# Kernel tuning notes

Hardware: AMD Instinct MI355X
Metric: run time of the kernel (lower is better)

Reference implementation:

```python
import jax, jax.numpy as jnp
import numpy as np

N = 50000
E = 1600000
IN_CH = 128
OUT_CH = 128
NEG_SLOPE = 0.2


def _gat_conv(x, W, att_src, att_dst, bias, src, dst, heads, out_ch, concat):
    # x: [N, F_in], W: [F_in, heads*out_ch], att_*: [heads, out_ch]
    n = x.shape[0]
    h = (x @ W).reshape(n, heads, out_ch)                    # [N, H, C]
    a_src = jnp.einsum('nhc,hc->nh', h, att_src)             # [N, H]
    a_dst = jnp.einsum('nhc,hc->nh', h, att_dst)             # [N, H]
    logits = jax.nn.leaky_relu(a_src[src] + a_dst[dst], NEG_SLOPE)  # [Etot, H]
    m = jax.ops.segment_max(logits, dst, num_segments=n)     # per-dst max (self-loops ensure non-empty)
    e = jnp.exp(logits - m[dst])
    denom = jax.ops.segment_sum(e, dst, num_segments=n)
    alpha = e / denom[dst]                                   # [Etot, H]
    msgs = h[src] * alpha[:, :, None]                        # [Etot, H, C]
    out = jax.ops.segment_sum(msgs, dst, num_segments=n)     # [N, H, C]
    out = out.reshape(n, heads * out_ch) if concat else out.mean(axis=1)
    return out + bias


def setup_inputs() -> dict:
    key = jax.random.key(0)
    ks = jax.random.split(key, 12)
    x = jax.random.normal(ks[0], (N, IN_CH), dtype=jnp.float32)
    edge_index = jax.random.randint(ks[1], (2, E), 0, N, dtype=jnp.int32)
    s = 0.1
    W_map = jax.random.normal(ks[2], (IN_CH, OUT_CH), dtype=jnp.float32) * s
    b_map = jnp.zeros((OUT_CH,), dtype=jnp.float32)
    # conv1: 128 -> 8 per head, 8 heads
    W1 = jax.random.normal(ks[3], (OUT_CH, 64), dtype=jnp.float32) * s
    att_src1 = jax.random.normal(ks[4], (8, 8), dtype=jnp.float32) * s
    att_dst1 = jax.random.normal(ks[5], (8, 8), dtype=jnp.float32) * s
    b1 = jnp.zeros((64,), dtype=jnp.float32)
    # conv2: 64 -> 128, 1 head, concat=False
    W2 = jax.random.normal(ks[6], (64, OUT_CH), dtype=jnp.float32) * s
    att_src2 = jax.random.normal(ks[7], (1, OUT_CH), dtype=jnp.float32) * s
    att_dst2 = jax.random.normal(ks[8], (1, OUT_CH), dtype=jnp.float32) * s
    b2 = jnp.zeros((OUT_CH,), dtype=jnp.float32)
    return {"x": x, "edge_index": edge_index, "W_map": W_map, "b_map": b_map,
            "W1": W1, "att_src1": att_src1, "att_dst1": att_dst1, "b1": b1,
            "W2": W2, "att_src2": att_src2, "att_dst2": att_dst2, "b2": b2}


def reference(x, edge_index, W_map, b_map, W1, att_src1, att_dst1, b1,
              W2, att_src2, att_dst2, b2):
    # add self-loops (PyG GATConv default)
    loops = jnp.arange(N, dtype=edge_index.dtype)
    src = jnp.concatenate([edge_index[0], loops])
    dst = jnp.concatenate([edge_index[1], loops])
    h = x @ W_map + b_map                                   # feature_mapping (dropout inactive in eval)
    h = _gat_conv(h, W1, att_src1, att_dst1, b1, src, dst, heads=8, out_ch=8, concat=True)
    h = jax.nn.elu(h)
    out = _gat_conv(h, W2, att_src2, att_dst2, b2, src, dst, heads=1, out_ch=OUT_CH, concat=False)
    return out
```

## Files before the change

kernel.cpp:

```cpp
#include <hip/hip_runtime.h>
#include <cstdint>
#include <cstddef>

#define NEG_SLOPE 0.2f
#define NBIN_MAX 1024
#define CAP_T 2560
#define SC_BLOCKS 512

typedef __attribute__((ext_vector_type(8))) short bf16x8;
typedef __attribute__((ext_vector_type(4))) float f32x4;

__device__ __forceinline__ float leaky(float x) { return x > 0.f ? x : NEG_SLOPE * x; }
__device__ __forceinline__ float blo(unsigned u) { return __uint_as_float(u << 16); }
__device__ __forceinline__ float bhi(unsigned u) { return __uint_as_float(u & 0xffff0000u); }
__device__ __forceinline__ unsigned short f2b(float f) {
    unsigned b = __float_as_uint(f);
    return (unsigned short)((b + 0x7fffu + ((b >> 16) & 1u)) >> 16);
}

__global__ void prep_kernel(const float* __restrict__ Wm, const float* __restrict__ W1,
                            const float* __restrict__ bm, const float* __restrict__ W2,
                            unsigned short* __restrict__ WcT, float* __restrict__ bc,
                            unsigned short* __restrict__ W2T, int* __restrict__ ccur,
                            int nbin) {
    int t = blockIdx.x * 256 + threadIdx.x;
    if (t < nbin) ccur[t] = 0;
    if (t < 8192) {
        int n = t >> 7, k = t & 127;
        float acc = 0.f;
        for (int c = 0; c < 128; c++) acc = fmaf(Wm[k * 128 + c], W1[c * 64 + n], acc);
        WcT[n * 128 + k] = f2b(acc);
        if (t < 64) {
            float a = 0.f;
            for (int c = 0; c < 128; c++) a = fmaf(bm[c], W1[c * 64 + t], a);
            bc[t] = a;
        }
    } else if (t < 16384) {
        int u = t - 8192;
        int n = u >> 6, k = u & 63;
        W2T[n * 64 + k] = f2b(W2[k * 128 + n]);
    }
}

__global__ __launch_bounds__(256) void phase2_kernel(
    const int* __restrict__ src, const int* __restrict__ dst, int E, int nbin,
    int* __restrict__ ccur, unsigned* __restrict__ tmp,
    const float* __restrict__ x, const unsigned short* __restrict__ WcT,
    const float* __restrict__ bc, const float* __restrict__ att_s,
    const float* __restrict__ att_d, unsigned short* __restrict__ h1b,
    float* __restrict__ as1, float* __restrict__ ad1, int N) {
    __shared__ int cnt[NBIN_MAX];
    if (blockIdx.x < SC_BLOCKS) {
        for (int i = threadIdx.x; i < nbin; i += 256) cnt[i] = 0;
        __syncthreads();
        int E4 = E >> 2;
        int chunk4 = (E4 + SC_BLOCKS - 1) / SC_BLOCKS;
        int b4 = blockIdx.x * chunk4;
        int e4 = b4 + chunk4; if (e4 > E4) e4 = E4;
        const int4* dst4 = (const int4*)dst;
        const int4* src4 = (const int4*)src;
        bool last = (blockIdx.x == SC_BLOCKS - 1);
        for (int i = b4 + threadIdx.x; i < e4; i += 256) {
            int4 d = dst4[i];
            atomicAdd(&cnt[d.x >> 6], 1);
            atomicAdd(&cnt[d.y >> 6], 1);
            atomicAdd(&cnt[d.z >> 6], 1);
            atomicAdd(&cnt[d.w >> 6], 1);
        }
        if (last)
            for (int i = (E4 << 2) + threadIdx.x; i < E; i += 256)
                atomicAdd(&cnt[dst[i] >> 6], 1);
        __syncthreads();
        for (int i = threadIdx.x; i < nbin; i += 256) {
            int c = cnt[i];
            cnt[i] = c ? atomicAdd(&ccur[i], c) : 0;
        }
        __syncthreads();
        for (int i = b4 + threadIdx.x; i < e4; i += 256) {
            int4 d = dst4[i];
            int4 s = src4[i];
#pragma unroll
            for (int k = 0; k < 4; k++) {
                int dd = (k == 0) ? d.x : (k == 1) ? d.y : (k == 2) ? d.z : d.w;
                int ss = (k == 0) ? s.x : (k == 1) ? s.y : (k == 2) ? s.z : s.w;
                int bin = dd >> 6;
                int p = atomicAdd(&cnt[bin], 1);
                if (p < CAP_T)
                    tmp[(size_t)bin * CAP_T + p] = ((unsigned)ss << 6) | (unsigned)(dd & 63);
            }
        }
        if (last)
            for (int i = (E4 << 2) + threadIdx.x; i < E; i += 256) {
                int dd = dst[i];
                int bin = dd >> 6;
                int p = atomicAdd(&cnt[bin], 1);
                if (p < CAP_T)
                    tmp[(size_t)bin * CAP_T + p] = ((unsigned)src[i] << 6) | (unsigned)(dd & 63);
            }
        return;
    }
    int wave = threadIdx.x >> 6, l = threadIdx.x & 63;
    int mtile = (blockIdx.x - SC_BLOCKS) * 4 + wave;
    int mtiles = N >> 4;
    if (mtile >= mtiles) return;
    int lm = l & 15, quad = l >> 4;
    const float* xr = x + ((size_t)(mtile * 16 + lm)) * 128 + quad * 8;
    f32x4 acc[4];
#pragma unroll
    for (int nt = 0; nt < 4; nt++) acc[nt] = (f32x4){0.f, 0.f, 0.f, 0.f};
#pragma unroll
    for (int kk = 0; kk < 4; kk++) {
        float4 xa = ((const float4*)(xr + kk * 32))[0];
        float4 xb = ((const float4*)(xr + kk * 32 + 4))[0];
        bf16x8 a;
        a[0] = (short)f2b(xa.x); a[1] = (short)f2b(xa.y);
        a[2] = (short)f2b(xa.z); a[3] = (short)f2b(xa.w);
        a[4] = (short)f2b(xb.x); a[5] = (short)f2b(xb.y);
        a[6] = (short)f2b(xb.z); a[7] = (short)f2b(xb.w);
#pragma unroll
        for (int nt = 0; nt < 4; nt++) {
            bf16x8 b = *(const bf16x8*)(WcT + (nt * 16 + lm) * 128 + kk * 32 + quad * 8);
            acc[nt] = __builtin_amdgcn_mfma_f32_16x16x32_bf16(a, b, acc[nt], 0, 0, 0);
        }
    }
    float vs[4][4], vd[4][4];
#pragma unroll
    for (int nt = 0; nt < 4; nt++) {
        int col = nt * 16 + lm;
        float sA = att_s[col], dA = att_d[col], bcv = bc[col];
#pragma unroll
        for (int r = 0; r < 4; r++) {
            float hv = acc[nt][r] + bcv;
            int row = mtile * 16 + quad * 4 + r;
            h1b[(size_t)row * 64 + col] = f2b(hv);
            vs[nt][r] = hv * sA;
            vd[nt][r] = hv * dA;
        }
    }
#pragma unroll
    for (int m = 1; m < 8; m <<= 1)
#pragma unroll
        for (int nt = 0; nt < 4; nt++)
#pragma unroll
            for (int r = 0; r < 4; r++) {
                vs[nt][r] += __shfl_xor(vs[nt][r], m);
                vd[nt][r] += __shfl_xor(vd[nt][r], m);
            }
    if ((lm & 7) == 0) {
        int hbase = lm >> 3;
#pragma unroll
        for (int nt = 0; nt < 4; nt++) {
            int H = 2 * nt + hbase;
#pragma unroll
            for (int r = 0; r < 4; r++) {
                int row = mtile * 16 + quad * 4 + r;
                as1[row * 8 + H] = vs[nt][r];
                ad1[row * 8 + H] = vd[nt][r];
            }
        }
    }
}

__global__ __launch_bounds__(256) void bin_finalize(
    const unsigned* __restrict__ tmp, const int* __restrict__ ccur,
    int* __restrict__ off, int* __restrict__ degv,
    unsigned short* __restrict__ bucket, int N) {
    __shared__ int cnt[64];
    __shared__ int cur[64];
    __shared__ unsigned short lbkt[CAP_T];
    int tid = threadIdx.x, b = blockIdx.x;
    if (tid < 64) cnt[tid] = 0;
    __syncthreads();
    int ecnt = ccur[b]; if (ecnt > CAP_T) ecnt = CAP_T;
    const unsigned* t = tmp + (size_t)b * CAP_T;
    const uint4* t4 = (const uint4*)t;
    int e4 = ecnt >> 2;
    for (int i = tid; i < e4; i += 256) {
        uint4 v = t4[i];
        atomicAdd(&cnt[v.x & 63u], 1);
        atomicAdd(&cnt[v.y & 63u], 1);
        atomicAdd(&cnt[v.z & 63u], 1);
        atomicAdd(&cnt[v.w & 63u], 1);
    }
    for (int i = (e4 << 2) + tid; i < ecnt; i += 256)
        atomicAdd(&cnt[t[i] & 63u], 1);
    __syncthreads();
    if (tid < 64) {
        int v = cnt[tid];
        int incl = v;
#pragma unroll
        for (int s = 1; s < 64; s <<= 1) {
            int u = __shfl_up(incl, s);
            if (tid >= s) incl += u;
        }
        int excl = incl - v;
        int node = b * 64 + tid;
        if (node < N) { off[node] = b * CAP_T + excl; degv[node] = v; }
        cur[tid] = excl;
    }
    __syncthreads();
    for (int i = tid; i < e4; i += 256) {
        uint4 v = t4[i];
        int p0 = atomicAdd(&cur[v.x & 63u], 1); lbkt[p0] = (unsigned short)(v.x >> 6);
        int p1 = atomicAdd(&cur[v.y & 63u], 1); lbkt[p1] = (unsigned short)(v.y >> 6);
        int p2 = atomicAdd(&cur[v.z & 63u], 1); lbkt[p2] = (unsigned short)(v.z >> 6);
        int p3 = atomicAdd(&cur[v.w & 63u], 1); lbkt[p3] = (unsigned short)(v.w >> 6);
    }
    for (int i = (e4 << 2) + tid; i < ecnt; i += 256) {
        unsigned u = t[i];
        int p = atomicAdd(&cur[u & 63u], 1);
        lbkt[p] = (unsigned short)(u >> 6);
    }
    __syncthreads();
    unsigned short* db = bucket + (size_t)b * CAP_T;
    int e8 = ecnt >> 3;
    uint4* d4 = (uint4*)db;
    const uint4* l4 = (const uint4*)lbkt;
    for (int i = tid; i < e8; i += 256) d4[i] = l4[i];
    for (int i = (e8 << 3) + tid; i < ecnt; i += 256) db[i] = lbkt[i];
}

__global__ __launch_bounds__(256) void conv1_agg(
    const int* __restrict__ off, const int* __restrict__ degv,
    const unsigned short* __restrict__ bucket,
    const unsigned* __restrict__ h1b, const float* __restrict__ as1,
    const float* __restrict__ ad1, const float* __restrict__ b1,
    unsigned* __restrict__ h1act, int N) {
    int wave = threadIdx.x >> 6, l = threadIdx.x & 63;
    int n = blockIdx.x * 4 + wave;
    if (n >= N) return;
    int begin = off[n];
    int deg = degv[n];
    int oo = l & 7, octet = l >> 3;
    unsigned qoff = (unsigned)(oo << 4);
    const char* h1c = (const char*)h1b;
    float adst = ad1[n * 8 + oo];
    float wself = __expf(leaky(as1[n * 8 + oo] + adst));
    float acc[8] = {0.f, 0.f, 0.f, 0.f, 0.f, 0.f, 0.f, 0.f};
    if (octet == 0) {
        uint4 us = *(const uint4*)(h1c + ((size_t)n << 7) + qoff);
        acc[0] = wself * blo(us.x); acc[1] = wself * bhi(us.x);
        acc[2] = wself * blo(us.y); acc[3] = wself * bhi(us.y);
        acc[4] = wself * blo(us.z); acc[5] = wself * bhi(us.z);
        acc[6] = wself * blo(us.w); acc[7] = wself * bhi(us.w);
    }
    float den_l = 0.f;
    unsigned sv[8]; float av[8];
#pragma unroll
    for (int j = 0; j < 8; j++) {
        int e = 8 * j + octet;
        sv[j] = (e < deg) ? (unsigned)bucket[begin + e] : 0u;
    }
#pragma unroll
    for (int j = 0; j < 8; j++) {
        float t = as1[sv[j] * 8 + oo];
        av[j] = (8 * j + octet < deg) ? t : -1e30f;
    }
    for (int c0 = 0; c0 < deg; c0 += 64) {
        uint4 uv[8];
#pragma unroll
        for (int j = 0; j < 8; j++) {
            uv[j] = make_uint4(0u, 0u, 0u, 0u);
            if (av[j] > -1e29f)
                uv[j] = *(const uint4*)(h1c + ((size_t)sv[j] << 7) + qoff);
        }
        int c1 = c0 + 64;
        bool more = c1 < deg;
        unsigned sn[8];
        if (more) {
#pragma unroll
            for (int j = 0; j < 8; j++) {
                int e = c1 + 8 * j + octet;
                sn[j] = (e < deg) ? (unsigned)bucket[begin + e] : 0u;
            }
        }
        float wv[8];
#pragma unroll
        for (int j = 0; j < 8; j++) {
            float w = __expf(leaky(av[j] + adst));
            wv[j] = w; den_l += w;
        }
        if (more) {
#pragma unroll
            for (int j = 0; j < 8; j++) {
                float t = as1[sn[j] * 8 + oo];
                av[j] = (c1 + 8 * j + octet < deg) ? t : -1e30f;
                sv[j] = sn[j];
            }
        }
#pragma unroll
        for (int j = 0; j < 8; j++) {
            acc[0] = fmaf(wv[j], blo(uv[j].x), acc[0]);
            acc[1] = fmaf(wv[j], bhi(uv[j].x), acc[1]);
            acc[2] = fmaf(wv[j], blo(uv[j].y), acc[2]);
            acc[3] = fmaf(wv[j], bhi(uv[j].y), acc[3]);
            acc[4] = fmaf(wv[j], blo(uv[j].z), acc[4]);
            acc[5] = fmaf(wv[j], bhi(uv[j].z), acc[5]);
            acc[6] = fmaf(wv[j], blo(uv[j].w), acc[6]);
            acc[7] = fmaf(wv[j], bhi(uv[j].w), acc[7]);
        }
    }
    den_l += __shfl_xor(den_l, 8);
    den_l += __shfl_xor(den_l, 16);
    den_l += __shfl_xor(den_l, 32);
    float den = den_l + wself;
#pragma unroll
    for (int i = 0; i < 8; i++) {
        acc[i] += __shfl_xor(acc[i], 8);
        acc[i] += __shfl_xor(acc[i], 16);
        acc[i] += __shfl_xor(acc[i], 32);
    }
    if (octet == 0) {
        float inv = 1.f / den;
        float4 b0 = ((const float4*)b1)[oo * 2];
        float4 b1v = ((const float4*)b1)[oo * 2 + 1];
        float o0 = acc[0] * inv + b0.x;
        float o1 = acc[1] * inv + b0.y;
        float o2 = acc[2] * inv + b0.z;
        float o3 = acc[3] * inv + b0.w;
        float o4 = acc[4] * inv + b1v.x;
        float o5 = acc[5] * inv + b1v.y;
        float o6 = acc[6] * inv + b1v.z;
        float o7 = acc[7] * inv + b1v.w;
        o0 = o0 > 0.f ? o0 : __expf(o0) - 1.f;
        o1 = o1 > 0.f ? o1 : __expf(o1) - 1.f;
        o2 = o2 > 0.f ? o2 : __expf(o2) - 1.f;
        o3 = o3 > 0.f ? o3 : __expf(o3) - 1.f;
        o4 = o4 > 0.f ? o4 : __expf(o4) - 1.f;
        o5 = o5 > 0.f ? o5 : __expf(o5) - 1.f;
        o6 = o6 > 0.f ? o6 : __expf(o6) - 1.f;
        o7 = o7 > 0.f ? o7 : __expf(o7) - 1.f;
        unsigned r0 = (unsigned)f2b(o0) | ((unsigned)f2b(o1) << 16);
        unsigned r1 = (unsigned)f2b(o2) | ((unsigned)f2b(o3) << 16);
        unsigned r2 = (unsigned)f2b(o4) | ((unsigned)f2b(o5) << 16);
        unsigned r3 = (unsigned)f2b(o6) | ((unsigned)f2b(o7) << 16);
        ((uint4*)h1act)[(size_t)n * 8 + oo] = make_uint4(r0, r1, r2, r3);
    }
}

__global__ __launch_bounds__(256) void gemm2_mfma(
    const unsigned short* __restrict__ h1act, const unsigned short* __restrict__ W2T,
    const float* __restrict__ att_s2, const float* __restrict__ att_d2,
    unsigned short* __restrict__ h2b, float* __restrict__ as2, float* __restrict__ ad2,
    int N) {
    int wave = threadIdx.x >> 6, l = threadIdx.x & 63;
    int mtile = blockIdx.x * 4 + wave;
    int mtiles = N >> 4;
    if (mtile >= mtiles) return;
    int lm = l & 15, quad = l >> 4;
    const unsigned short* ar = h1act + (size_t)(mtile * 16 + lm) * 64 + quad * 8;
    bf16x8 a0 = *(const bf16x8*)(ar);
    bf16x8 a1 = *(const bf16x8*)(ar + 32);
    f32x4 acc[8];
#pragma unroll
    for (int nt = 0; nt < 8; nt++) acc[nt] = (f32x4){0.f, 0.f, 0.f, 0.f};
#pragma unroll
    for (int nt = 0; nt < 8; nt++) {
        const unsigned short* br = W2T + (nt * 16 + lm) * 64 + quad * 8;
        bf16x8 b0 = *(const bf16x8*)(br);
        bf16x8 b1v = *(const bf16x8*)(br + 32);
        acc[nt] = __builtin_amdgcn_mfma_f32_16x16x32_bf16(a0, b0, acc[nt], 0, 0, 0);
        acc[nt] = __builtin_amdgcn_mfma_f32_16x16x32_bf16(a1, b1v, acc[nt], 0, 0, 0);
    }
    float vs[4] = {0.f, 0.f, 0.f, 0.f}, vd[4] = {0.f, 0.f, 0.f, 0.f};
#pragma unroll
    for (int nt = 0; nt < 8; nt++) {
        int col = nt * 16 + lm;
        float sA = att_s2[col], dA = att_d2[col];
#pragma unroll
        for (int r = 0; r < 4; r++) {
            float hv = acc[nt][r];
            int row = mtile * 16 + quad * 4 + r;
            h2b[(size_t)row * 128 + col] = f2b(hv);
            vs[r] = fmaf(hv, sA, vs[r]);
            vd[r] = fmaf(hv, dA, vd[r]);
        }
    }
#pragma unroll
    for (int m = 1; m < 16; m <<= 1)
#pragma unroll
        for (int r = 0; r < 4; r++) {
            vs[r] += __shfl_xor(vs[r], m);
            vd[r] += __shfl_xor(vd[r], m);
        }
    if (lm == 0) {
#pragma unroll
        for (int r = 0; r < 4; r++) {
            int row = mtile * 16 + quad * 4 + r;
            as2[row] = vs[r];
            ad2[row] = vd[r];
        }
    }
}

__global__ __launch_bounds__(256) void conv2_agg(
    const int* __restrict__ off, const int* __restrict__ degv,
    const unsigned short* __restrict__ bucket,
    const unsigned* __restrict__ h2b, const float* __restrict__ as2,
    const float* __restrict__ ad2, const float* __restrict__ b2,
    float* __restrict__ out, int N) {
    int wave = threadIdx.x >> 6, l = threadIdx.x & 63;
    int n = blockIdx.x * 4 + wave;
    if (n >= N) return;
    int begin = off[n];
    int deg = degv[n];
    int qq = l & 15, quarter = l >> 4;
    unsigned qoff = (unsigned)(qq << 4);
    const char* h2c = (const char*)h2b;
    float adst = ad2[n];
    float wself = __expf(leaky(as2[n] + adst));
    float acc[8] = {0.f, 0.f, 0.f, 0.f, 0.f, 0.f, 0.f, 0.f};
    if (quarter == 0) {
        uint4 us = *(const uint4*)(h2c + ((size_t)n << 8) + qoff);
        acc[0] = wself * blo(us.x); acc[1] = wself * bhi(us.x);
        acc[2] = wself * blo(us.y); acc[3] = wself * bhi(us.y);
        acc[4] = wself * blo(us.z); acc[5] = wself * bhi(us.z);
        acc[6] = wself * blo(us.w); acc[7] = wself * bhi(us.w);
    }
    float den_l = 0.f;
    unsigned sv[8]; float av[8];
#pragma unroll
    for (int j = 0; j < 8; j++) {
        int e = 4 * j + quarter;
        sv[j] = (e < deg) ? (unsigned)bucket[begin + e] : 0u;
    }
#pragma unroll
    for (int j = 0; j < 8; j++) {
        float t = as2[sv[j]];
        av[j] = (4 * j + quarter < deg) ? t : -1e30f;
    }
    for (int c0 = 0; c0 < deg; c0 += 32) {
        uint4 uv[8];
#pragma unroll
        for (int j = 0; j < 8; j++) {
            uv[j] = make_uint4(0u, 0u, 0u, 0u);
            if (av[j] > -1e29f)
                uv[j] = *(const uint4*)(h2c + ((size_t)sv[j] << 8) + qoff);
        }
        int c1 = c0 + 32;
        bool more = c1 < deg;
        unsigned sn[8];
        if (more) {
#pragma unroll
            for (int j = 0; j < 8; j++) {
                int e = c1 + 4 * j + quarter;
                sn[j] = (e < deg) ? (unsigned)bucket[begin + e] : 0u;
            }
        }
        float wv[8];
#pragma unroll
        for (int j = 0; j < 8; j++) {
            float w = __expf(leaky(av[j] + adst));
            wv[j] = w; den_l += w;
        }
        if (more) {
#pragma unroll
            for (int j = 0; j < 8; j++) {
                float t = as2[sn[j]];
                av[j] = (c1 + 4 * j + quarter < deg) ? t : -1e30f;
                sv[j] = sn[j];
            }
        }
#pragma unroll
        for (int j = 0; j < 8; j++) {
            acc[0] = fmaf(wv[j], blo(uv[j].x), acc[0]);
            acc[1] = fmaf(wv[j], bhi(uv[j].x), acc[1]);
            acc[2] = fmaf(wv[j], blo(uv[j].y), acc[2]);
            acc[3] = fmaf(wv[j], bhi(uv[j].y), acc[3]);
            acc[4] = fmaf(wv[j], blo(uv[j].z), acc[4]);
            acc[5] = fmaf(wv[j], bhi(uv[j].z), acc[5]);
            acc[6] = fmaf(wv[j], blo(uv[j].w), acc[6]);
            acc[7] = fmaf(wv[j], bhi(uv[j].w), acc[7]);
        }
    }
    den_l += __shfl_xor(den_l, 16);
    den_l += __shfl_xor(den_l, 32);
    float den = den_l + wself;
#pragma unroll
    for (int i = 0; i < 8; i++) {
        acc[i] += __shfl_xor(acc[i], 16);
        acc[i] += __shfl_xor(acc[i], 32);
    }
    if (quarter == 0) {
        float inv = 1.f / den;
        float4 b0 = ((const float4*)b2)[qq * 2];
        float4 b1v = ((const float4*)b2)[qq * 2 + 1];
        ((float4*)out)[(size_t)n * 32 + qq * 2] = make_float4(
            acc[0] * inv + b0.x, acc[1] * inv + b0.y,
            acc[2] * inv + b0.z, acc[3] * inv + b0.w);
        ((float4*)out)[(size_t)n * 32 + qq * 2 + 1] = make_float4(
            acc[4] * inv + b1v.x, acc[5] * inv + b1v.y,
            acc[6] * inv + b1v.z, acc[7] * inv + b1v.w);
    }
}

extern "C" void kernel_launch(void* const* d_in, const int* in_sizes, int n_in,
                              void* d_out, int out_size, void* d_ws, size_t ws_size,
                              hipStream_t stream) {
    const float* x   = (const float*)d_in[0];
    const int*   ei  = (const int*)d_in[1];
    const float* Wm  = (const float*)d_in[2];
    const float* bm  = (const float*)d_in[3];
    const float* W1  = (const float*)d_in[4];
    const float* As1 = (const float*)d_in[5];
    const float* Ad1 = (const float*)d_in[6];
    const float* b1  = (const float*)d_in[7];
    const float* W2  = (const float*)d_in[8];
    const float* As2 = (const float*)d_in[9];
    const float* Ad2 = (const float*)d_in[10];
    const float* b2  = (const float*)d_in[11];
    int N = in_sizes[0] / 128;
    int E = in_sizes[1] / 2;
    const int* srcv = ei;
    const int* dstv = ei + E;

    char* p = (char*)d_ws;
    auto alloc = [&](size_t bytes) {
        void* r = (void*)p;
        p += (bytes + 255) & ~(size_t)255;
        return r;
    };
    int nbin = (N + 63) / 64;
    int*   degv   = (int*)alloc((size_t)N * 4);
    int*   off    = (int*)alloc((size_t)N * 4);
    int*   ccur   = (int*)alloc((size_t)nbin * 4);
    unsigned short* bucket = (unsigned short*)alloc((size_t)nbin * CAP_T * 2);
    unsigned short* WcT  = (unsigned short*)alloc(64 * 128 * 2);
    float*          bc   = (float*)alloc(64 * 4);
    unsigned short* W2T  = (unsigned short*)alloc(128 * 64 * 2);
    unsigned short* h1b  = (unsigned short*)alloc((size_t)N * 64 * 2);
    float* a_s1   = (float*)alloc((size_t)N * 8 * 4);
    float* a_d1   = (float*)alloc((size_t)N * 8 * 4);
    unsigned* h1act = (unsigned*)alloc((size_t)N * 64 * 2);
    unsigned short* h2b = (unsigned short*)alloc((size_t)N * 128 * 2);
    unsigned* tmp = (unsigned*)h2b;
    float* a_s2   = (float*)alloc((size_t)N * 4);
    float* a_d2   = (float*)alloc((size_t)N * 4);
    float* outp   = (float*)d_out;

    int mtiles = N >> 4;
    int gemm_blocks = (mtiles + 3) / 4;
    prep_kernel<<<64, 256, 0, stream>>>(Wm, W1, bm, W2, WcT, bc, W2T, ccur, nbin);
    phase2_kernel<<<SC_BLOCKS + gemm_blocks, 256, 0, stream>>>(
        srcv, dstv, E, nbin, ccur, tmp, x, WcT, bc, As1, Ad1, h1b, a_s1, a_d1, N);
    bin_finalize<<<nbin, 256, 0, stream>>>(tmp, ccur, off, degv, bucket, N);
    conv1_agg<<<(N + 3) / 4, 256, 0, stream>>>(off, degv, bucket, (const unsigned*)h1b, a_s1, a_d1, b1, h1act, N);
    gemm2_mfma<<<(mtiles + 3) / 4, 256, 0, stream>>>((const unsigned short*)h1act, W2T, As2, Ad2, h2b, a_s2, a_d2, N);
    conv2_agg<<<(N + 3) / 4, 256, 0, stream>>>(off, degv, bucket, (const unsigned*)h2b, a_s2, a_d2, b2, outp, N);
}
```

Baseline: 277.8 us.

## Compute conv2 edge weights wave-wide into LDS and double-buffer gathers

```diff
diff --git a/kernel.cpp b/kernel.cpp
--- a/kernel.cpp
+++ b/kernel.cpp
@@ -249,7 +249,8 @@
 #pragma unroll
     for (int j = 0; j < 8; j++) {
         int e = 8 * j + octet;
-        sv[j] = (e < deg) ? (unsigned)bucket[begin + e] : 0u;
+        unsigned sraw = (unsigned)bucket[begin + e];
+        sv[j] = (e < deg) ? sraw : 0u;
     }
 #pragma unroll
     for (int j = 0; j < 8; j++) {
@@ -259,11 +260,8 @@
     for (int c0 = 0; c0 < deg; c0 += 64) {
         uint4 uv[8];
 #pragma unroll
-        for (int j = 0; j < 8; j++) {
-            uv[j] = make_uint4(0u, 0u, 0u, 0u);
-            if (av[j] > -1e29f)
-                uv[j] = *(const uint4*)(h1c + ((size_t)sv[j] << 7) + qoff);
-        }
+        for (int j = 0; j < 8; j++)
+            uv[j] = *(const uint4*)(h1c + ((size_t)sv[j] << 7) + qoff);
         int c1 = c0 + 64;
         bool more = c1 < deg;
         unsigned sn[8];
@@ -271,7 +269,8 @@
 #pragma unroll
             for (int j = 0; j < 8; j++) {
                 int e = c1 + 8 * j + octet;
-                sn[j] = (e < deg) ? (unsigned)bucket[begin + e] : 0u;
+                unsigned sraw = (unsigned)bucket[begin + e];
+                sn[j] = (e < deg) ? sraw : 0u;
             }
         }
         float wv[8];
@@ -399,6 +398,7 @@
     const unsigned* __restrict__ h2b, const float* __restrict__ as2,
     const float* __restrict__ ad2, const float* __restrict__ b2,
     float* __restrict__ out, int N) {
+    __shared__ uint2 ew[4][64];
     int wave = threadIdx.x >> 6, l = threadIdx.x & 63;
     int n = blockIdx.x * 4 + wave;
     if (n >= N) return;
@@ -417,64 +417,59 @@
         acc[4] = wself * blo(us.z); acc[5] = wself * bhi(us.z);
         acc[6] = wself * blo(us.w); acc[7] = wself * bhi(us.w);
     }
+    uint2 wA[4], wB[4];
+    uint4 uA[4], uB[4];
+    auto loadg = [&](uint2 (&pw)[4], uint4 (&uv)[4], int g) {
+#pragma unroll
+        for (int k = 0; k < 4; k++) {
+            pw[k] = ew[wave][16 * g + 4 * k + quarter];
+            uv[k] = *(const uint4*)(h2c + pw[k].y + qoff);
+        }
+    };
+    auto fmag = [&](uint2 (&pw)[4], uint4 (&uv)[4]) {
+#pragma unroll
+        for (int k = 0; k < 4; k++) {
+            float w_ = __uint_as_float(pw[k].x);
+            acc[0] = fmaf(w_, blo(uv[k].x), acc[0]);
+            acc[1] = fmaf(w_, bhi(uv[k].x), acc[1]);
+            acc[2] = fmaf(w_, blo(uv[k].y), acc[2]);
+            acc[3] = fmaf(w_, bhi(uv[k].y), acc[3]);
+            acc[4] = fmaf(w_, blo(uv[k].z), acc[4]);
+            acc[5] = fmaf(w_, bhi(uv[k].z), acc[5]);
+            acc[6] = fmaf(w_, blo(uv[k].w), acc[6]);
+            acc[7] = fmaf(w_, bhi(uv[k].w), acc[7]);
+        }
+    };
     float den_l = 0.f;
-    unsigned sv[8]; float av[8];
-#pragma unroll
-    for (int j = 0; j < 8; j++) {
-        int e = 4 * j + quarter;
-        sv[j] = (e < deg) ? (unsigned)bucket[begin + e] : 0u;
-    }
-#pragma unroll
-    for (int j = 0; j < 8; j++) {
-        float t = as2[sv[j]];
-        av[j] = (4 * j + quarter < deg) ? t : -1e30f;
-    }
-    for (int c0 = 0; c0 < deg; c0 += 32) {
-        uint4 uv[8];
-#pragma unroll
-        for (int j = 0; j < 8; j++) {
-            uv[j] = make_uint4(0u, 0u, 0u, 0u);
-            if (av[j] > -1e29f)
-                uv[j] = *(const uint4*)(h2c + ((size_t)sv[j] << 8) + qoff);
-        }
-        int c1 = c0 + 32;
-        bool more = c1 < deg;
-        unsigned sn[8];
-        if (more) {
-#pragma unroll
-            for (int j = 0; j < 8; j++) {
-                int e = c1 + 4 * j + quarter;
-                sn[j] = (e < deg) ? (unsigned)bucket[begin + e] : 0u;
-            }
-        }
-        float wv[8];
-#pragma unroll
-        for (int j = 0; j < 8; j++) {
-            float w = __expf(leaky(av[j] + adst));
-            wv[j] = w; den_l += w;
-        }
-        if (more) {
-#pragma unroll
-            for (int j = 0; j < 8; j++) {
-                float t = as2[sn[j]];
-                av[j] = (c1 + 4 * j + quarter < deg) ? t : -1e30f;
-                sv[j] = sn[j];
-            }
-        }
-#pragma unroll
-        for (int j = 0; j < 8; j++) {
-            acc[0] = fmaf(wv[j], blo(uv[j].x), acc[0]);
-            acc[1] = fmaf(wv[j], bhi(uv[j].x), acc[1]);
-            acc[2] = fmaf(wv[j], blo(uv[j].y), acc[2]);
-            acc[3] = fmaf(wv[j], bhi(uv[j].y), acc[3]);
-            acc[4] = fmaf(wv[j], blo(uv[j].z), acc[4]);
-            acc[5] = fmaf(wv[j], bhi(uv[j].z), acc[5]);
-            acc[6] = fmaf(wv[j], blo(uv[j].w), acc[6]);
-            acc[7] = fmaf(wv[j], bhi(uv[j].w), acc[7]);
-        }
-    }
-    den_l += __shfl_xor(den_l, 16);
-    den_l += __shfl_xor(den_l, 32);
+    for (int c0 = 0; c0 < deg; c0 += 64) {
+        int j = c0 + l;
+        unsigned sraw = (unsigned)bucket[begin + j];
+        unsigned s = (j < deg) ? sraw : 0u;
+        float a = as2[s];
+        a = (j < deg) ? a : -1e30f;
+        float w = __expf(leaky(a + adst));
+        den_l += w;
+        ew[wave][l] = make_uint2(__float_as_uint(w), s << 8);
+        int cend = deg - c0; if (cend > 64) cend = 64;
+        int ng = (cend + 15) >> 4;
+        loadg(wA, uA, 0);
+        int g = 1;
+        for (; g + 1 < ng; g += 2) {
+            loadg(wB, uB, g);
+            fmag(wA, uA);
+            loadg(wA, uA, g + 1);
+            fmag(wB, uB);
+        }
+        if (g < ng) {
+            loadg(wB, uB, g);
+            fmag(wA, uA);
+            fmag(wB, uB);
+        } else {
+            fmag(wA, uA);
+        }
+    }
+#pragma unroll
+    for (int s = 1; s < 64; s <<= 1) den_l += __shfl_xor(den_l, s);
     float den = den_l + wself;
 #pragma unroll
     for (int i = 0; i < 8; i++) {
```

After: 270.2 us. -2.7%, faster.
